# Performance work log

Measured on AMD Instinct MI355X. Metric: run time of the kernel, lower is better.

The kernel has to match this reference:

```python
import jax, jax.numpy as jnp
import numpy as np

EPS = 1e-6

def _phi(x):
    # elu(x) + 1 feature map
    return jax.nn.elu(x) + 1.0

def setup_inputs() -> dict:
    key = jax.random.key(0)
    kq, kk, kv = jax.random.split(key, 3)
    N, L, S, H, D, M = 8, 4096, 4096, 8, 64, 64
    queries = jax.random.normal(kq, (N, L, H, D), dtype=jnp.float32)
    keys = jax.random.normal(kk, (N, S, H, D), dtype=jnp.float32)
    values = jax.random.normal(kv, (N, S, H, M), dtype=jnp.float32)
    key_mask = jnp.ones((N, S), dtype=jnp.float32)  # key_lengths.float_matrix
    return {"queries": queries, "keys": keys, "values": values, "key_mask": key_mask}

def reference(queries, keys, values, key_mask):
    Q = _phi(queries)                                   # [N,L,H,D]
    K = _phi(keys) * key_mask[:, :, None, None]         # [N,S,H,D]
    KV = jnp.einsum('nshd,nshm->nhmd', K, values)       # [N,H,M,D]
    Z = 1.0 / (jnp.einsum('nlhd,nhd->nlh', Q, K.sum(axis=1)) + EPS)  # [N,L,H]
    V = jnp.einsum('nlhd,nhmd,nlh->nlhm', Q, KV, Z)     # [N,L,H,M]
    return V
```

## Files before the change

kernel.cpp:

```cpp
#include <hip/hip_runtime.h>


#define SLEN 4096
#define LLEN 4096
#define NHTOT 64
#define HD   512
#define NSPLIT 8
#define EPSF 1e-6f

__device__ __forceinline__ float phi(float x) {
    return x > 0.0f ? x + 1.0f : __expf(x);
}

__device__ __forceinline__ void fma4(float4& a, float s, const float4& b) {
    a.x = fmaf(s, b.x, a.x);
    a.y = fmaf(s, b.y, a.y);
    a.z = fmaf(s, b.z, a.z);
    a.w = fmaf(s, b.w, a.w);
}

__global__ __launch_bounds__(256, 2)
void la_phase1(const float* __restrict__ Kg, const float* __restrict__ Vg,
               const float* __restrict__ maskg,
               float* __restrict__ KVp, float* __restrict__ Ksump) {
    __shared__ float smem[4][4096];
    __shared__ float ksb[16 * 64];

    const int tid  = threadIdx.x;
    const int w    = tid >> 6;
    const int lane = tid & 63;
    const int nh   = blockIdx.y;
    const int n    = nh >> 3;
    const int h    = nh & 7;
    const int sp   = blockIdx.x;

    const int sr4 = lane >> 4;
    const int c4  = (lane & 15) * 4;
    const int d0  = (lane & 7) * 8;
    const int m0  = (lane >> 3) * 8;

    float* kw = smem[w];
    float* vw = smem[w] + 2048;

    const size_t base = (size_t)n * SLEN * HD + (size_t)h * 64;
    const float* mrow = maskg + (size_t)n * SLEN;
    const int wrow0 = sp * 512 + w * 128;

    float4 acc[8][2];
    #pragma unroll
    for (int i = 0; i < 8; ++i) {
        acc[i][0] = make_float4(0.f, 0.f, 0.f, 0.f);
        acc[i][1] = make_float4(0.f, 0.f, 0.f, 0.f);
    }
    float4 ksp = make_float4(0.f, 0.f, 0.f, 0.f);

    float4 pk[8], pv[8];
    float  pm[8];
    #pragma unroll
    for (int u = 0; u < 8; ++u) {
        const int s = wrow0 + sr4 + u * 4;
        const size_t g = base + (size_t)s * HD + c4;
        pk[u] = *(const float4*)(Kg + g);
        pv[u] = *(const float4*)(Vg + g);
        pm[u] = mrow[s];
    }

    #pragma unroll
    for (int t = 0; t < 4; ++t) {
        #pragma unroll
        for (int u = 0; u < 8; ++u) {
            const int row = sr4 + u * 4;
            float4 kf = pk[u];
            const float mm = pm[u];
            kf.x = phi(kf.x) * mm;
            kf.y = phi(kf.y) * mm;
            kf.z = phi(kf.z) * mm;
            kf.w = phi(kf.w) * mm;
            ksp.x += kf.x; ksp.y += kf.y; ksp.z += kf.z; ksp.w += kf.w;
            *(float4*)&kw[row * 64 + c4] = kf;
            *(float4*)&vw[row * 64 + c4] = pv[u];
        }
        if (t < 3) {
            #pragma unroll
            for (int u = 0; u < 8; ++u) {
                const int s = wrow0 + (t + 1) * 32 + sr4 + u * 4;
                const size_t g = base + (size_t)s * HD + c4;
                pk[u] = *(const float4*)(Kg + g);
                pv[u] = *(const float4*)(Vg + g);
                pm[u] = mrow[s];
            }
        }
        #pragma unroll 4
        for (int s = 0; s < 32; ++s) {
            const float4 ka = *(const float4*)&kw[s * 64 + d0];
            const float4 kz = *(const float4*)&kw[s * 64 + d0 + 4];
            const float4 va = *(const float4*)&vw[s * 64 + m0];
            const float4 vz = *(const float4*)&vw[s * 64 + m0 + 4];
            fma4(acc[0][0], ka.x, va); fma4(acc[0][1], ka.x, vz);
            fma4(acc[1][0], ka.y, va); fma4(acc[1][1], ka.y, vz);
            fma4(acc[2][0], ka.z, va); fma4(acc[2][1], ka.z, vz);
            fma4(acc[3][0], ka.w, va); fma4(acc[3][1], ka.w, vz);
            fma4(acc[4][0], kz.x, va); fma4(acc[4][1], kz.x, vz);
            fma4(acc[5][0], kz.y, va); fma4(acc[5][1], kz.y, vz);
            fma4(acc[6][0], kz.z, va); fma4(acc[6][1], kz.z, vz);
            fma4(acc[7][0], kz.w, va); fma4(acc[7][1], kz.w, vz);
        }
    }

    *(float4*)&ksb[(w * 4 + sr4) * 64 + c4] = ksp;

    #pragma unroll
    for (int di = 0; di < 8; ++di) {
        *(float4*)&smem[w][(d0 + di) * 64 + m0]     = acc[di][0];
        *(float4*)&smem[w][(d0 + di) * 64 + m0 + 4] = acc[di][1];
    }
    __syncthreads();

    float* outp = KVp + ((size_t)sp * NHTOT + nh) * 4096;
    #pragma unroll
    for (int j = 0; j < 4; ++j) {
        const int f = (j * 256 + tid) * 4;
        float4 a  = *(const float4*)&smem[0][f];
        const float4 b1 = *(const float4*)&smem[1][f];
        const float4 b2 = *(const float4*)&smem[2][f];
        const float4 b3 = *(const float4*)&smem[3][f];
        a.x += b1.x + b2.x + b3.x;
        a.y += b1.y + b2.y + b3.y;
        a.z += b1.z + b2.z + b3.z;
        a.w += b1.w + b2.w + b3.w;
        *(float4*)&outp[f] = a;
    }
    if (tid < 64) {
        float ssum = 0.f;
        #pragma unroll
        for (int r = 0; r < 16; ++r) ssum += ksb[r * 64 + tid];
        Ksump[((size_t)sp * NHTOT + nh) * 64 + tid] = ssum;
    }
}

__global__ __launch_bounds__(256)
void la_reduce(const float* __restrict__ KVp, const float* __restrict__ Ksump,
               float* __restrict__ KVt, float* __restrict__ Ksum) {
    const int nh  = blockIdx.x >> 2;
    const int j   = blockIdx.x & 3;
    const int tid = threadIdx.x;
    const int f = (j * 256 + tid) * 4;
    float4 a = make_float4(0.f, 0.f, 0.f, 0.f);
    #pragma unroll
    for (int s = 0; s < NSPLIT; ++s) {
        const float4 v = *(const float4*)&KVp[((size_t)s * NHTOT + nh) * 4096 + f];
        a.x += v.x; a.y += v.y; a.z += v.z; a.w += v.w;
    }
    *(float4*)&KVt[(size_t)nh * 4096 + f] = a;
    if (j == 0 && tid < 64) {
        float b = 0.f;
        #pragma unroll
        for (int s = 0; s < NSPLIT; ++s)
            b += Ksump[((size_t)s * NHTOT + nh) * 64 + tid];
        Ksum[nh * 64 + tid] = b;
    }
}

__global__ __launch_bounds__(256, 2)
void la_phase2(const float* __restrict__ Qg, const float* __restrict__ KVt,
               const float* __restrict__ Ksum, float* __restrict__ Og) {
    __shared__ float Qs[256 * 64];
    __shared__ float KVs[64 * 64];

    const int tid = threadIdx.x;
    const int nh  = blockIdx.y;
    const int n   = nh >> 3;
    const int h   = nh & 7;
    const int lbase = blockIdx.x * 256;

    #pragma unroll
    for (int j = 0; j < 4; ++j) {
        const int f = (j * 256 + tid) * 4;
        *(float4*)&KVs[f] = *(const float4*)&KVt[(size_t)nh * 4096 + f];
    }

    const int sr = tid >> 4;
    const int cc = tid & 15;
    #pragma unroll
    for (int u = 0; u < 16; ++u) {
        const int row = u * 16 + sr;
        float4 q = *(const float4*)&Qg[((size_t)(n * LLEN + lbase + row) * 8 + h) * 64 + cc * 4];
        q.x = phi(q.x); q.y = phi(q.y); q.z = phi(q.z); q.w = phi(q.w);
        *(float4*)&Qs[row * 64 + (cc ^ (row & 7)) * 4] = q;
    }
    __syncthreads();

    const int w    = tid >> 6;
    const int lane = tid & 63;
    const int ty   = lane >> 3;
    const int tx   = lane & 7;
    const int m0   = tx * 8;
    const int rb   = w * 64 + ty;

    float4 acc[8][2];
    float  den[8];
    #pragma unroll
    for (int i = 0; i < 8; ++i) {
        acc[i][0] = make_float4(0.f, 0.f, 0.f, 0.f);
        acc[i][1] = make_float4(0.f, 0.f, 0.f, 0.f);
        den[i] = 0.f;
    }

    const float* ksrow = Ksum + nh * 64;

    for (int d4 = 0; d4 < 16; ++d4) {
        const float4 ks = *(const float4*)&ksrow[d4 * 4];
        float4 q4[8];
        #pragma unroll
        for (int i = 0; i < 8; ++i)
            q4[i] = *(const float4*)&Qs[(rb + 8 * i) * 64 + ((d4 ^ ty) * 4)];
        #pragma unroll
        for (int i = 0; i < 8; ++i) {
            den[i] = fmaf(q4[i].x, ks.x, den[i]);
            den[i] = fmaf(q4[i].y, ks.y, den[i]);
            den[i] = fmaf(q4[i].z, ks.z, den[i]);
            den[i] = fmaf(q4[i].w, ks.w, den[i]);
        }
        #pragma unroll
        for (int dk = 0; dk < 4; ++dk) {
            const float4 kva = *(const float4*)&KVs[(d4 * 4 + dk) * 64 + m0];
            const float4 kvz = *(const float4*)&KVs[(d4 * 4 + dk) * 64 + m0 + 4];
            #pragma unroll
            for (int i = 0; i < 8; ++i) {
                const float qv = (&q4[i].x)[dk];
                fma4(acc[i][0], qv, kva);
                fma4(acc[i][1], qv, kvz);
            }
        }
    }

    #pragma unroll
    for (int i = 0; i < 8; ++i) {
        const int l = lbase + rb + 8 * i;
        const float z = 1.0f / (den[i] + EPSF);
        float4 o0 = acc[i][0], o1 = acc[i][1];
        o0.x *= z; o0.y *= z; o0.z *= z; o0.w *= z;
        o1.x *= z; o1.y *= z; o1.z *= z; o1.w *= z;
        float* op = &Og[((size_t)(n * LLEN + l) * 8 + h) * 64 + m0];
        *(float4*)op       = o0;
        *(float4*)(op + 4) = o1;
    }
}

extern "C" void kernel_launch(void* const* d_in, const int* in_sizes, int n_in,
                              void* d_out, int out_size, void* d_ws, size_t ws_size,
                              hipStream_t stream) {
    const float* Q    = (const float*)d_in[0];
    const float* K    = (const float*)d_in[1];
    const float* V    = (const float*)d_in[2];
    const float* mask = (const float*)d_in[3];
    float* out = (float*)d_out;

    float* KVp   = (float*)d_ws;
    float* Ksump = KVp + (size_t)NSPLIT * NHTOT * 4096;
    float* KVt   = Ksump + (size_t)NSPLIT * NHTOT * 64;
    float* Ksum  = KVt + (size_t)NHTOT * 4096;

    dim3 g1(NSPLIT, NHTOT);
    la_phase1<<<g1, 256, 0, stream>>>(K, V, mask, KVp, Ksump);

    la_reduce<<<256, 256, 0, stream>>>(KVp, Ksump, KVt, Ksum);

    dim3 g2(LLEN / 256, NHTOT);
    la_phase2<<<g2, 256, 0, stream>>>(Q, KVt, Ksum, out);
}
```

Baseline: 262.1 us.

## Use split-bf16 MFMA for phase2 Q·KV product with transposed bf16 KV

Phase2 now computes the Q·KV product with bf16 MFMA instructions. Each fp32 operand is split into hi and lo bf16 parts, and three MFMAs per tile keep accuracy close to fp32. The reduce kernel now writes KV transposed as hi/lo bf16 arrays through a small LDS transpose. Phase2 drops its Q and KV shared-memory staging and reads Q straight from global into registers. The aim is to take the FMA-bound phase2 onto the matrix cores, at the cost of extra split arithmetic, some precision loss and scattered scalar output stores.

```diff
diff --git a/kernel.cpp b/kernel.cpp
--- a/kernel.cpp
+++ b/kernel.cpp
@@ -8,6 +8,9 @@
 #define NSPLIT 8
 #define EPSF 1e-6f
 
+typedef short s16x8 __attribute__((ext_vector_type(8)));
+typedef float f32x4 __attribute__((ext_vector_type(4)));
+
 __device__ __forceinline__ float phi(float x) {
     return x > 0.0f ? x + 1.0f : __expf(x);
 }
@@ -17,6 +20,13 @@
     a.y = fmaf(s, b.y, a.y);
     a.z = fmaf(s, b.z, a.z);
     a.w = fmaf(s, b.w, a.w);
+}
+
+__device__ __forceinline__ void bsplit(float x, short& hi, short& lo) {
+    const unsigned bx = __float_as_uint(x);
+    hi = (short)(bx >> 16);
+    const float hf = __uint_as_float(bx & 0xFFFF0000u);
+    lo = (short)(__float_as_uint(x - hf) >> 16);
 }
 
 __global__ __launch_bounds__(256, 2)
@@ -140,19 +150,36 @@
 
 __global__ __launch_bounds__(256)
 void la_reduce(const float* __restrict__ KVp, const float* __restrict__ Ksump,
-               float* __restrict__ KVt, float* __restrict__ Ksum) {
-    const int nh  = blockIdx.x >> 2;
-    const int j   = blockIdx.x & 3;
+               short* __restrict__ KVThi, short* __restrict__ KVTlo,
+               float* __restrict__ Ksum) {
+    __shared__ float ld[64 * 20];
+
+    const int nh  = blockIdx.y;
+    const int mb  = blockIdx.x * 16;
     const int tid = threadIdx.x;
-    const int f = (j * 256 + tid) * 4;
+
+    const int d    = tid >> 2;
+    const int moff = (tid & 3) * 4;
     float4 a = make_float4(0.f, 0.f, 0.f, 0.f);
     #pragma unroll
     for (int s = 0; s < NSPLIT; ++s) {
-        const float4 v = *(const float4*)&KVp[((size_t)s * NHTOT + nh) * 4096 + f];
+        const float4 v = *(const float4*)&KVp[((size_t)s * NHTOT + nh) * 4096 + d * 64 + mb + moff];
         a.x += v.x; a.y += v.y; a.z += v.z; a.w += v.w;
     }
-    *(float4*)&KVt[(size_t)nh * 4096 + f] = a;
-    if (j == 0 && tid < 64) {
+    *(float4*)&ld[d * 20 + moff] = a;
+    __syncthreads();
+
+    const int mloc = tid >> 4;
+    const int d0   = (tid & 15) * 4;
+    short hi4[4], lo4[4];
+    #pragma unroll
+    for (int i = 0; i < 4; ++i)
+        bsplit(ld[(d0 + i) * 20 + mloc], hi4[i], lo4[i]);
+    const size_t o = (size_t)nh * 4096 + (mb + mloc) * 64 + d0;
+    *(short4*)&KVThi[o] = *(short4*)hi4;
+    *(short4*)&KVTlo[o] = *(short4*)lo4;
+
+    if (blockIdx.x == 0 && tid < 64) {
         float b = 0.f;
         #pragma unroll
         for (int s = 0; s < NSPLIT; ++s)
@@ -161,89 +188,101 @@
     }
 }
 
-__global__ __launch_bounds__(256, 2)
-void la_phase2(const float* __restrict__ Qg, const float* __restrict__ KVt,
+__global__ __launch_bounds__(256)
+void la_phase2(const float* __restrict__ Qg,
+               const short* __restrict__ KVThi, const short* __restrict__ KVTlo,
                const float* __restrict__ Ksum, float* __restrict__ Og) {
-    __shared__ float Qs[256 * 64];
-    __shared__ float KVs[64 * 64];
-
-    const int tid = threadIdx.x;
-    const int nh  = blockIdx.y;
-    const int n   = nh >> 3;
-    const int h   = nh & 7;
-    const int lbase = blockIdx.x * 256;
-
-    #pragma unroll
-    for (int j = 0; j < 4; ++j) {
-        const int f = (j * 256 + tid) * 4;
-        *(float4*)&KVs[f] = *(const float4*)&KVt[(size_t)nh * 4096 + f];
-    }
-
-    const int sr = tid >> 4;
-    const int cc = tid & 15;
-    #pragma unroll
-    for (int u = 0; u < 16; ++u) {
-        const int row = u * 16 + sr;
-        float4 q = *(const float4*)&Qg[((size_t)(n * LLEN + lbase + row) * 8 + h) * 64 + cc * 4];
-        q.x = phi(q.x); q.y = phi(q.y); q.z = phi(q.z); q.w = phi(q.w);
-        *(float4*)&Qs[row * 64 + (cc ^ (row & 7)) * 4] = q;
-    }
-    __syncthreads();
-
+    const int tid  = threadIdx.x;
     const int w    = tid >> 6;
     const int lane = tid & 63;
-    const int ty   = lane >> 3;
-    const int tx   = lane & 7;
-    const int m0   = tx * 8;
-    const int rb   = w * 64 + ty;
-
-    float4 acc[8][2];
-    float  den[8];
-    #pragma unroll
-    for (int i = 0; i < 8; ++i) {
-        acc[i][0] = make_float4(0.f, 0.f, 0.f, 0.f);
-        acc[i][1] = make_float4(0.f, 0.f, 0.f, 0.f);
-        den[i] = 0.f;
-    }
-
-    const float* ksrow = Ksum + nh * 64;
-
-    for (int d4 = 0; d4 < 16; ++d4) {
-        const float4 ks = *(const float4*)&ksrow[d4 * 4];
-        float4 q4[8];
-        #pragma unroll
-        for (int i = 0; i < 8; ++i)
-            q4[i] = *(const float4*)&Qs[(rb + 8 * i) * 64 + ((d4 ^ ty) * 4)];
-        #pragma unroll
-        for (int i = 0; i < 8; ++i) {
-            den[i] = fmaf(q4[i].x, ks.x, den[i]);
-            den[i] = fmaf(q4[i].y, ks.y, den[i]);
-            den[i] = fmaf(q4[i].z, ks.z, den[i]);
-            den[i] = fmaf(q4[i].w, ks.w, den[i]);
-        }
-        #pragma unroll
-        for (int dk = 0; dk < 4; ++dk) {
-            const float4 kva = *(const float4*)&KVs[(d4 * 4 + dk) * 64 + m0];
-            const float4 kvz = *(const float4*)&KVs[(d4 * 4 + dk) * 64 + m0 + 4];
+    const int nh   = blockIdx.y;
+    const int n    = nh >> 3;
+    const int h    = nh & 7;
+    const int l0   = blockIdx.x * 128 + w * 32;
+
+    const int r  = lane & 15;
+    const int g4 = lane >> 4;
+
+    const short* bhp = KVThi + (size_t)nh * 4096;
+    const short* blp = KVTlo + (size_t)nh * 4096;
+    const float* ksp = Ksum + nh * 64;
+
+    f32x4 acc[2][4];
+    #pragma unroll
+    for (int t = 0; t < 2; ++t)
+        #pragma unroll
+        for (int u = 0; u < 4; ++u)
+            acc[t][u] = (f32x4){0.f, 0.f, 0.f, 0.f};
+    float den[2] = {0.f, 0.f};
+
+    #pragma unroll
+    for (int g = 0; g < 2; ++g) {
+        const int db = g * 32 + g4 * 8;
+
+        s16x8 Bh[4], Bl[4];
+        #pragma unroll
+        for (int u = 0; u < 4; ++u) {
+            Bh[u] = *(const s16x8*)&bhp[(u * 16 + r) * 64 + db];
+            Bl[u] = *(const s16x8*)&blp[(u * 16 + r) * 64 + db];
+        }
+        const float4 k0 = *(const float4*)&ksp[db];
+        const float4 k1 = *(const float4*)&ksp[db + 4];
+
+        #pragma unroll
+        for (int t = 0; t < 2; ++t) {
+            const float* qrow = Qg + ((size_t)(n * LLEN + l0 + t * 16 + r) * 8 + h) * 64 + db;
+            float4 q0 = *(const float4*)qrow;
+            float4 q1 = *(const float4*)(qrow + 4);
+            q0.x = phi(q0.x); q0.y = phi(q0.y); q0.z = phi(q0.z); q0.w = phi(q0.w);
+            q1.x = phi(q1.x); q1.y = phi(q1.y); q1.z = phi(q1.z); q1.w = phi(q1.w);
+
+            float dn = den[t];
+            dn = fmaf(q0.x, k0.x, dn); dn = fmaf(q0.y, k0.y, dn);
+            dn = fmaf(q0.z, k0.z, dn); dn = fmaf(q0.w, k0.w, dn);
+            dn = fmaf(q1.x, k1.x, dn); dn = fmaf(q1.y, k1.y, dn);
+            dn = fmaf(q1.z, k1.z, dn); dn = fmaf(q1.w, k1.w, dn);
+            den[t] = dn;
+
+            s16x8 Ah, Al;
+            {
+                short hh, ll;
+                bsplit(q0.x, hh, ll); Ah[0] = hh; Al[0] = ll;
+                bsplit(q0.y, hh, ll); Ah[1] = hh; Al[1] = ll;
+                bsplit(q0.z, hh, ll); Ah[2] = hh; Al[2] = ll;
+                bsplit(q0.w, hh, ll); Ah[3] = hh; Al[3] = ll;
+                bsplit(q1.x, hh, ll); Ah[4] = hh; Al[4] = ll;
+                bsplit(q1.y, hh, ll); Ah[5] = hh; Al[5] = ll;
+                bsplit(q1.z, hh, ll); Ah[6] = hh; Al[6] = ll;
+                bsplit(q1.w, hh, ll); Ah[7] = hh; Al[7] = ll;
+            }
             #pragma unroll
-            for (int i = 0; i < 8; ++i) {
-                const float qv = (&q4[i].x)[dk];
-                fma4(acc[i][0], qv, kva);
-                fma4(acc[i][1], qv, kvz);
+            for (int u = 0; u < 4; ++u) {
+                acc[t][u] = __builtin_amdgcn_mfma_f32_16x16x32_bf16(Ah, Bh[u], acc[t][u], 0, 0, 0);
+                acc[t][u] = __builtin_amdgcn_mfma_f32_16x16x32_bf16(Ah, Bl[u], acc[t][u], 0, 0, 0);
+                acc[t][u] = __builtin_amdgcn_mfma_f32_16x16x32_bf16(Al, Bh[u], acc[t][u], 0, 0, 0);
             }
         }
     }
 
     #pragma unroll
-    for (int i = 0; i < 8; ++i) {
-        const int l = lbase + rb + 8 * i;
-        const float z = 1.0f / (den[i] + EPSF);
-        float4 o0 = acc[i][0], o1 = acc[i][1];
-        o0.x *= z; o0.y *= z; o0.z *= z; o0.w *= z;
-        o1.x *= z; o1.y *= z; o1.z *= z; o1.w *= z;
-        float* op = &Og[((size_t)(n * LLEN + l) * 8 + h) * 64 + m0];
-        *(float4*)op       = o0;
-        *(float4*)(op + 4) = o1;
+    for (int t = 0; t < 2; ++t) {
+        den[t] += __shfl_xor(den[t], 16, 64);
+        den[t] += __shfl_xor(den[t], 32, 64);
+    }
+
+    #pragma unroll
+    for (int t = 0; t < 2; ++t) {
+        #pragma unroll
+        for (int k = 0; k < 4; ++k) {
+            const int ro = g4 * 4 + k;
+            const float dk = __shfl(den[t], ro, 64);
+            const float z  = 1.0f / (dk + EPSF);
+            const int l = l0 + t * 16 + ro;
+            float* op = &Og[((size_t)(n * LLEN + l) * 8 + h) * 64 + r];
+            #pragma unroll
+            for (int u = 0; u < 4; ++u)
+                op[u * 16] = acc[t][u][k] * z;
+        }
     }
 }
 
@@ -258,14 +297,16 @@
 
     float* KVp   = (float*)d_ws;
     float* Ksump = KVp + (size_t)NSPLIT * NHTOT * 4096;
-    float* KVt   = Ksump + (size_t)NSPLIT * NHTOT * 64;
-    float* Ksum  = KVt + (size_t)NHTOT * 4096;
+    float* Ksum  = Ksump + (size_t)NSPLIT * NHTOT * 64;
+    short* KVThi = (short*)(Ksum + NHTOT * 64);
+    short* KVTlo = KVThi + (size_t)NHTOT * 4096;
 
     dim3 g1(NSPLIT, NHTOT);
     la_phase1<<<g1, 256, 0, stream>>>(K, V, mask, KVp, Ksump);
 
-    la_reduce<<<256, 256, 0, stream>>>(KVp, Ksump, KVt, Ksum);
-
-    dim3 g2(LLEN / 256, NHTOT);
-    la_phase2<<<g2, 256, 0, stream>>>(Q, KVt, Ksum, out);
-}
+    dim3 gr(4, NHTOT);
+    la_reduce<<<gr, 256, 0, stream>>>(KVp, Ksump, KVThi, KVTlo, Ksum);
+
+    dim3 g2(LLEN / 128, NHTOT);
+    la_phase2<<<g2, 256, 0, stream>>>(Q, KVThi, KVTlo, Ksum, out);
+}
```

Result: faster. 249.7 us (-4.7%).
